# Kernel optimization log

Hardware: AMD Instinct MI355X
Metric: run time of the kernel (lower is better)

Reference implementation:

```python
import jax, jax.numpy as jnp
import numpy as np

N_NODES = 100000
N_EDGES = 600000
N_FEAT = 128


def setup_inputs() -> dict:
    key = jax.random.key(0)
    k1, k2, k3 = jax.random.split(key, 3)
    x = jax.random.normal(k1, (N_NODES, N_FEAT), dtype=jnp.float32)
    W = jax.random.normal(k2, (N_FEAT, N_FEAT), dtype=jnp.float32) / np.sqrt(N_FEAT)
    b = jnp.zeros((N_FEAT,), dtype=jnp.float32)
    edge_index = jax.random.randint(k3, (2, N_EDGES), 0, N_NODES, dtype=jnp.int64)
    return {"x": x, "W": W, "b": b, "edge_index": edge_index}


def reference(x, W, b, edge_index):
    # GCNConv: out = D^{-1/2} (A + I) D^{-1/2} (x @ W) + b, then ReLU
    n = x.shape[0]
    loop = jnp.arange(n, dtype=edge_index.dtype)
    src = jnp.concatenate([edge_index[0], loop])  # [E + N]
    dst = jnp.concatenate([edge_index[1], loop])  # [E + N]

    # degree of target nodes (includes self-loops)
    ones = jnp.ones(src.shape[0], dtype=x.dtype)
    deg = jax.ops.segment_sum(ones, dst, num_segments=n)  # [N]
    dinv = jnp.where(deg > 0, jax.lax.rsqrt(deg), 0.0)
    norm = dinv[src] * dinv[dst]  # [E + N]

    h = x @ W  # [N, F]
    msg = h[src] * norm[:, None]  # gather + scale, [E + N, F]
    agg = jax.ops.segment_sum(msg, dst, num_segments=n)  # scatter-add, [N, F]
    return jax.nn.relu(agg + b)
```

## Files before the change

kernel.cpp:

```cpp
#include <hip/hip_runtime.h>

#define NN 100000
#define NE 600000
#define F  128
#define CAP 32

#define NBLK   ((NN + 255) / 256)
#define GEMM_B ((NN + 127) / 128)
#define FILL_B ((NE + 2047) / 2048)

#define OFF_DEG  0
#define OFF_FLAG (960*1024)
#define OFF_WT   (1024*1024)
#define OFF_G    (2048*1024)
#define OFF_CSR  (28672*1024)

typedef __attribute__((ext_vector_type(8))) short bf16x8;
typedef __attribute__((ext_vector_type(16))) float f32x16;
typedef __attribute__((ext_vector_type(4)))  float f32x4;

__device__ inline unsigned short f2b(float f) {
    unsigned int u = __builtin_bit_cast(unsigned int, f);
    u += 0x7fffu + ((u >> 16) & 1u);
    return (unsigned short)(u >> 16);
}
__device__ inline float b_lo(unsigned int v) {
    return __builtin_bit_cast(float, v << 16);
}
__device__ inline float b_hi(unsigned int v) {
    return __builtin_bit_cast(float, v & 0xffff0000u);
}
__device__ inline void acc8(float* a, uint4 v, float d) {
    a[0] += b_lo(v.x) * d; a[1] += b_hi(v.x) * d;
    a[2] += b_lo(v.y) * d; a[3] += b_hi(v.y) * d;
    a[4] += b_lo(v.z) * d; a[5] += b_hi(v.z) * d;
    a[6] += b_lo(v.w) * d; a[7] += b_hi(v.w) * d;
}

__global__ __launch_bounds__(256) void k_init(const int* __restrict__ ei,
                                              const float* __restrict__ W,
                                              int* __restrict__ deg,
                                              int* __restrict__ flag,
                                              unsigned short* __restrict__ pb) {
    int i = blockIdx.x * 256 + threadIdx.x;
    if (i < NN) deg[i] = 0;
    if (i < F * F) {
        int j  = i & 7;
        int l  = (i >> 3) & 63;
        int tt = i >> 9;
        int k  = (tt >> 2) * 16 + ((l >> 5) << 3) + j;
        int n  = (tt & 3) * 32 + (l & 31);
        pb[i] = f2b(W[k * F + n]);
    }
    if (blockIdx.x == 0) {
        __shared__ int cnt;
        if (threadIdx.x == 0) cnt = 0;
        __syncthreads();
        if (ei[2 * threadIdx.x + 1] == 0) atomicAdd(&cnt, 1);
        __syncthreads();
        if (threadIdx.x == 0) *flag = (cnt > 128) ? 1 : 0;
    }
}

__global__ __launch_bounds__(256) void k_gemm_fill(const float* __restrict__ x,
                                                   const unsigned short* __restrict__ pb,
                                                   unsigned short* __restrict__ gb,
                                                   const int* __restrict__ ei,
                                                   const int* __restrict__ flag,
                                                   int* __restrict__ deg,
                                                   int* __restrict__ csr) {
    if (blockIdx.x < FILL_B) {
        const int base = blockIdx.x * 2048 + threadIdx.x;
        if (*flag) {
            const uint2* e64 = (const uint2*)ei;
#pragma unroll
            for (int i = 0; i < 8; ++i) {
                int e = base + i * 256;
                if (e < NE) {
                    int src = (int)e64[e].x;
                    int dst = (int)e64[NE + e].x;
                    int slot = atomicAdd(&deg[dst], 1);
                    if (slot < CAP) csr[slot * NN + dst] = src;
                }
            }
        } else {
#pragma unroll
            for (int i = 0; i < 8; ++i) {
                int e = base + i * 256;
                if (e < NE) {
                    int src = ei[e];
                    int dst = ei[NE + e];
                    int slot = atomicAdd(&deg[dst], 1);
                    if (slot < CAP) csr[slot * NN + dst] = src;
                }
            }
        }
        return;
    }

    __shared__ unsigned short xs[128 * 128];
    const int t    = threadIdx.x;
    const int row0 = (blockIdx.x - FILL_B) * 128;

#pragma unroll 4
    for (int it = 0; it < 16; ++it) {
        int r  = it * 8 + (t >> 5);
        int gr = min(row0 + r, NN - 1);
        float4 v = *(const float4*)(x + (long)gr * F + (t & 31) * 4);
        unsigned int lo = (unsigned int)f2b(v.x) | ((unsigned int)f2b(v.y) << 16);
        unsigned int hi = (unsigned int)f2b(v.z) | ((unsigned int)f2b(v.w) << 16);
        int bcol = ((t & 31) * 8) ^ ((r & 15) << 4);
        uint2 u; u.x = lo; u.y = hi;
        *(uint2*)((char*)xs + r * 256 + bcol) = u;
    }
    __syncthreads();

    const int w    = t >> 6;
    const int lane = t & 63;
    const int m    = lane & 31;
    const int half = lane >> 5;

    f32x16 acc[4];
#pragma unroll
    for (int nt = 0; nt < 4; ++nt)
#pragma unroll
        for (int j = 0; j < 16; ++j) acc[nt][j] = 0.f;

    const int r = 32 * w + m;
    const unsigned short* pw = pb + lane * 8;

#pragma unroll
    for (int kc = 0; kc < 8; ++kc) {
        int bcol = (kc * 32 + half * 16) ^ ((r & 15) << 4);
        bf16x8 a = *(const bf16x8*)((const char*)xs + r * 256 + bcol);
#pragma unroll
        for (int nt = 0; nt < 4; ++nt) {
            bf16x8 bfr = *(const bf16x8*)(pw + (kc * 4 + nt) * 512);
            acc[nt] = __builtin_amdgcn_mfma_f32_32x32x16_bf16(a, bfr, acc[nt], 0, 0, 0);
        }
    }
    __syncthreads();

    const int rbase = 32 * w + 4 * half;
#pragma unroll
    for (int nt = 0; nt < 4; ++nt) {
#pragma unroll
        for (int reg = 0; reg < 16; ++reg) {
            int row = rbase + (reg & 3) + 8 * (reg >> 2);
            int cb  = (nt * 32 + m) * 2;
            *(unsigned short*)((char*)xs + row * 256 + (cb ^ ((row & 15) << 4))) =
                f2b(acc[nt][reg]);
        }
    }
    __syncthreads();

#pragma unroll
    for (int p = 0; p < 8; ++p) {
        int row  = p * 16 + (t >> 4);
        int cb   = (t & 15) * 16;
        uint4 v  = *(const uint4*)((const char*)xs + row * 256 + (cb ^ ((row & 15) << 4)));
        int grow = row0 + row;
        if (grow < NN)
            *(uint4*)((char*)gb + (long)grow * 256 + cb) = v;
    }
}

__global__ __launch_bounds__(256) void k_gather(const int* __restrict__ deg,
                                                const int* __restrict__ csr,
                                                const unsigned short* __restrict__ gb,
                                                const float* __restrict__ b,
                                                float* __restrict__ out) {
    int n = blockIdx.x * 4 + (threadIdx.x >> 6);
    if (n >= NN) return;
    const int lane = threadIdx.x & 63;
    const int l16  = lane & 15;
    const int grp  = lane >> 4;
    const int dn   = deg[n];
    const int dnc  = min(dn, CAP);
    const float dvn = rsqrtf((float)(dn + 1));

    float a[8];
    if (grp == 0) {
        uint4 v = *(const uint4*)(gb + (long)n * F + l16 * 8);
        a[0] = b_lo(v.x) * dvn; a[1] = b_hi(v.x) * dvn;
        a[2] = b_lo(v.y) * dvn; a[3] = b_hi(v.y) * dvn;
        a[4] = b_lo(v.z) * dvn; a[5] = b_hi(v.z) * dvn;
        a[6] = b_lo(v.w) * dvn; a[7] = b_hi(v.w) * dvn;
    } else {
#pragma unroll
        for (int j = 0; j < 8; ++j) a[j] = 0.f;
    }

    const int p0 = grp, p1 = grp + 4, p2 = grp + 8, p3 = grp + 12;
    int s0 = n, s1 = n, s2 = n, s3 = n;
    if (p0 < dnc) s0 = csr[p0 * NN + n];
    if (p1 < dnc) s1 = csr[p1 * NN + n];
    if (p2 < dnc) s2 = csr[p2 * NN + n];
    if (p3 < dnc) s3 = csr[p3 * NN + n];
    uint4 z; z.x = z.y = z.z = z.w = 0u;
    uint4 v0 = z, v1 = z, v2 = z, v3 = z;
    if (p0 < dnc) v0 = *(const uint4*)(gb + (long)s0 * F + l16 * 8);
    if (p1 < dnc) v1 = *(const uint4*)(gb + (long)s1 * F + l16 * 8);
    if (p2 < dnc) v2 = *(const uint4*)(gb + (long)s2 * F + l16 * 8);
    if (p3 < dnc) v3 = *(const uint4*)(gb + (long)s3 * F + l16 * 8);
    float d0 = rsqrtf((float)(deg[s0] + 1));
    float d1 = rsqrtf((float)(deg[s1] + 1));
    float d2 = rsqrtf((float)(deg[s2] + 1));
    float d3 = rsqrtf((float)(deg[s3] + 1));
    acc8(a, v0, d0);
    acc8(a, v1, d1);
    acc8(a, v2, d2);
    acc8(a, v3, d3);

    for (int p = grp + 16; p < dnc; p += 4) {
        int s = csr[p * NN + n];
        float d = rsqrtf((float)(deg[s] + 1));
        uint4 v = *(const uint4*)(gb + (long)s * F + l16 * 8);
        acc8(a, v, d);
    }

#pragma unroll
    for (int j = 0; j < 8; ++j) {
        a[j] += __shfl_xor(a[j], 16);
        a[j] += __shfl_xor(a[j], 32);
    }

    if (grp == 0) {
        float4 b0 = *(const float4*)(b + l16 * 8);
        float4 b1 = *(const float4*)(b + l16 * 8 + 4);
        f32x4 o0, o1;
        o0[0] = fmaxf(a[0] * dvn + b0.x, 0.f);
        o0[1] = fmaxf(a[1] * dvn + b0.y, 0.f);
        o0[2] = fmaxf(a[2] * dvn + b0.z, 0.f);
        o0[3] = fmaxf(a[3] * dvn + b0.w, 0.f);
        o1[0] = fmaxf(a[4] * dvn + b1.x, 0.f);
        o1[1] = fmaxf(a[5] * dvn + b1.y, 0.f);
        o1[2] = fmaxf(a[6] * dvn + b1.z, 0.f);
        o1[3] = fmaxf(a[7] * dvn + b1.w, 0.f);
        long obase = (long)n * F + l16 * 8;
        __builtin_nontemporal_store(o0, (f32x4*)(out + obase));
        __builtin_nontemporal_store(o1, (f32x4*)(out + obase + 4));
    }
}

extern "C" void kernel_launch(void* const* d_in, const int* in_sizes, int n_in,
                              void* d_out, int out_size, void* d_ws, size_t ws_size,
                              hipStream_t stream) {
    const float* x  = (const float*)d_in[0];
    const float* W  = (const float*)d_in[1];
    const float* b  = (const float*)d_in[2];
    const int*   ei = (const int*)d_in[3];
    float* out = (float*)d_out;

    char* ws = (char*)d_ws;
    int*            deg  = (int*)(ws + OFF_DEG);
    int*            flag = (int*)(ws + OFF_FLAG);
    unsigned short* pb   = (unsigned short*)(ws + OFF_WT);
    unsigned short* gb   = (unsigned short*)(ws + OFF_G);
    int*            csr  = (int*)(ws + OFF_CSR);

    k_init<<<NBLK, 256, 0, stream>>>(ei, W, deg, flag, pb);
    k_gemm_fill<<<FILL_B + GEMM_B, 256, 0, stream>>>(x, pb, gb, ei, flag, deg, csr);
    k_gather<<<(NN + 3) / 4, 256, 0, stream>>>(deg, csr, gb, b, out);
}
```

Baseline: 179.0 us.

## Fuse init, gemm/fill and gather into one cooperative persistent kernel

Merges the three kernel launches into a single cooperative kernel that uses grid-wide syncs between the init, fill/GEMM and gather phases. Blocks loop over virtual block indices in a persistent style, with the grid sized from an occupancy query. The goal is to remove launch gaps and tail drain between kernels. The cost is grid.sync overhead, a grid capped by occupancy (256 per CU assumed) and possibly lower latency hiding in the gather phase. It falls back to the three-kernel path if the cooperative launch fails.

```diff
diff --git a/kernel.cpp b/kernel.cpp
--- a/kernel.cpp
+++ b/kernel.cpp
@@ -1,4 +1,7 @@
 #include <hip/hip_runtime.h>
+#include <hip/hip_cooperative_groups.h>
+
+namespace cg = cooperative_groups;
 
 #define NN 100000
 #define NE 600000
@@ -8,6 +11,8 @@
 #define NBLK   ((NN + 255) / 256)
 #define GEMM_B ((NN + 127) / 128)
 #define FILL_B ((NE + 2047) / 2048)
+#define PH1_B  (FILL_B + GEMM_B)
+#define GATH_B ((NN + 3) / 4)
 
 #define OFF_DEG  0
 #define OFF_FLAG (960*1024)
@@ -37,14 +42,13 @@
     a[6] += b_lo(v.w) * d; a[7] += b_hi(v.w) * d;
 }
 
-__global__ __launch_bounds__(256) void k_init(const int* __restrict__ ei,
-                                              const float* __restrict__ W,
-                                              int* __restrict__ deg,
-                                              int* __restrict__ flag,
-                                              unsigned short* __restrict__ pb) {
-    int i = blockIdx.x * 256 + threadIdx.x;
-    if (i < NN) deg[i] = 0;
-    if (i < F * F) {
+
+__device__ __forceinline__ void init_body(const float* __restrict__ W,
+                                          int* __restrict__ deg,
+                                          unsigned short* __restrict__ pb,
+                                          int gtid, int gstride) {
+    for (int i = gtid; i < NN; i += gstride) deg[i] = 0;
+    for (int i = gtid; i < F * F; i += gstride) {
         int j  = i & 7;
         int l  = (i >> 3) & 63;
         int tt = i >> 9;
@@ -52,55 +56,44 @@
         int n  = (tt & 3) * 32 + (l & 31);
         pb[i] = f2b(W[k * F + n]);
     }
-    if (blockIdx.x == 0) {
-        __shared__ int cnt;
-        if (threadIdx.x == 0) cnt = 0;
-        __syncthreads();
-        if (ei[2 * threadIdx.x + 1] == 0) atomicAdd(&cnt, 1);
-        __syncthreads();
-        if (threadIdx.x == 0) *flag = (cnt > 128) ? 1 : 0;
-    }
-}
-
-__global__ __launch_bounds__(256) void k_gemm_fill(const float* __restrict__ x,
-                                                   const unsigned short* __restrict__ pb,
-                                                   unsigned short* __restrict__ gb,
-                                                   const int* __restrict__ ei,
-                                                   const int* __restrict__ flag,
-                                                   int* __restrict__ deg,
-                                                   int* __restrict__ csr) {
-    if (blockIdx.x < FILL_B) {
-        const int base = blockIdx.x * 2048 + threadIdx.x;
-        if (*flag) {
-            const uint2* e64 = (const uint2*)ei;
-#pragma unroll
-            for (int i = 0; i < 8; ++i) {
-                int e = base + i * 256;
-                if (e < NE) {
-                    int src = (int)e64[e].x;
-                    int dst = (int)e64[NE + e].x;
-                    int slot = atomicAdd(&deg[dst], 1);
-                    if (slot < CAP) csr[slot * NN + dst] = src;
-                }
+}
+
+__device__ __forceinline__ void fill_body(int fb, const int* __restrict__ ei,
+                                          int f64, int* __restrict__ deg,
+                                          int* __restrict__ csr) {
+    const int base = fb * 2048 + threadIdx.x;
+    if (f64) {
+        const uint2* e64 = (const uint2*)ei;
+#pragma unroll
+        for (int i = 0; i < 8; ++i) {
+            int e = base + i * 256;
+            if (e < NE) {
+                int src = (int)e64[e].x;
+                int dst = (int)e64[NE + e].x;
+                int slot = atomicAdd(&deg[dst], 1);
+                if (slot < CAP) csr[slot * NN + dst] = src;
             }
-        } else {
-#pragma unroll
-            for (int i = 0; i < 8; ++i) {
-                int e = base + i * 256;
-                if (e < NE) {
-                    int src = ei[e];
-                    int dst = ei[NE + e];
-                    int slot = atomicAdd(&deg[dst], 1);
-                    if (slot < CAP) csr[slot * NN + dst] = src;
-                }
+        }
+    } else {
+#pragma unroll
+        for (int i = 0; i < 8; ++i) {
+            int e = base + i * 256;
+            if (e < NE) {
+                int src = ei[e];
+                int dst = ei[NE + e];
+                int slot = atomicAdd(&deg[dst], 1);
+                if (slot < CAP) csr[slot * NN + dst] = src;
             }
         }
-        return;
-    }
-
-    __shared__ unsigned short xs[128 * 128];
+    }
+}
+
+__device__ __forceinline__ void gemm_body(int gbi, const float* __restrict__ x,
+                                          const unsigned short* __restrict__ pb,
+                                          unsigned short* __restrict__ gb,
+                                          unsigned short* xs) {
     const int t    = threadIdx.x;
-    const int row0 = (blockIdx.x - FILL_B) * 128;
+    const int row0 = gbi * 128;
 
 #pragma unroll 4
     for (int it = 0; it < 16; ++it) {
@@ -163,14 +156,15 @@
         if (grow < NN)
             *(uint4*)((char*)gb + (long)grow * 256 + cb) = v;
     }
-}
-
-__global__ __launch_bounds__(256) void k_gather(const int* __restrict__ deg,
-                                                const int* __restrict__ csr,
-                                                const unsigned short* __restrict__ gb,
-                                                const float* __restrict__ b,
-                                                float* __restrict__ out) {
-    int n = blockIdx.x * 4 + (threadIdx.x >> 6);
+    __syncthreads();
+}
+
+__device__ __forceinline__ void gather_body(int vb, const int* __restrict__ deg,
+                                            const int* __restrict__ csr,
+                                            const unsigned short* __restrict__ gb,
+                                            const float* __restrict__ b,
+                                            float* __restrict__ out) {
+    int n = vb * 4 + (threadIdx.x >> 6);
     if (n >= NN) return;
     const int lane = threadIdx.x & 63;
     const int l16  = lane & 15;
@@ -243,6 +237,79 @@
     }
 }
 
+__global__ __launch_bounds__(256) void k_fused(const float* __restrict__ x,
+                                               const float* __restrict__ W,
+                                               const float* __restrict__ b,
+                                               const int* __restrict__ ei,
+                                               float* __restrict__ out,
+                                               int* __restrict__ deg,
+                                               int* __restrict__ flag,
+                                               unsigned short* __restrict__ pb,
+                                               unsigned short* __restrict__ gb,
+                                               int* __restrict__ csr) {
+    __shared__ unsigned short xs[128 * 128];
+    cg::grid_group grid = cg::this_grid();
+    const int gtid    = blockIdx.x * 256 + threadIdx.x;
+    const int gstride = gridDim.x * 256;
+
+    init_body(W, deg, pb, gtid, gstride);
+    if (blockIdx.x == 0) {
+        __shared__ int cnt;
+        if (threadIdx.x == 0) cnt = 0;
+        __syncthreads();
+        if (ei[2 * threadIdx.x + 1] == 0) atomicAdd(&cnt, 1);
+        __syncthreads();
+        if (threadIdx.x == 0) *flag = (cnt > 128) ? 1 : 0;
+    }
+    grid.sync();
+
+    const int f64 = *flag;
+    for (int v = blockIdx.x; v < PH1_B; v += gridDim.x) {
+        if (v < FILL_B) fill_body(v, ei, f64, deg, csr);
+        else            gemm_body(v - FILL_B, x, pb, gb, xs);
+    }
+    grid.sync();
+
+    for (int v = blockIdx.x; v < GATH_B; v += gridDim.x)
+        gather_body(v, deg, csr, gb, b, out);
+}
+
+__global__ __launch_bounds__(256) void k_init(const int* __restrict__ ei,
+                                              const float* __restrict__ W,
+                                              int* __restrict__ deg,
+                                              int* __restrict__ flag,
+                                              unsigned short* __restrict__ pb) {
+    init_body(W, deg, pb, blockIdx.x * 256 + threadIdx.x, NBLK * 256);
+    if (blockIdx.x == 0) {
+        __shared__ int cnt;
+        if (threadIdx.x == 0) cnt = 0;
+        __syncthreads();
+        if (ei[2 * threadIdx.x + 1] == 0) atomicAdd(&cnt, 1);
+        __syncthreads();
+        if (threadIdx.x == 0) *flag = (cnt > 128) ? 1 : 0;
+    }
+}
+
+__global__ __launch_bounds__(256) void k_gemm_fill(const float* __restrict__ x,
+                                                   const unsigned short* __restrict__ pb,
+                                                   unsigned short* __restrict__ gb,
+                                                   const int* __restrict__ ei,
+                                                   const int* __restrict__ flag,
+                                                   int* __restrict__ deg,
+                                                   int* __restrict__ csr) {
+    __shared__ unsigned short xs[128 * 128];
+    if (blockIdx.x < FILL_B) fill_body(blockIdx.x, ei, *flag, deg, csr);
+    else                     gemm_body(blockIdx.x - FILL_B, x, pb, gb, xs);
+}
+
+__global__ __launch_bounds__(256) void k_gather(const int* __restrict__ deg,
+                                                const int* __restrict__ csr,
+                                                const unsigned short* __restrict__ gb,
+                                                const float* __restrict__ b,
+                                                float* __restrict__ out) {
+    gather_body(blockIdx.x, deg, csr, gb, b, out);
+}
+
 extern "C" void kernel_launch(void* const* d_in, const int* in_sizes, int n_in,
                               void* d_out, int out_size, void* d_ws, size_t ws_size,
                               hipStream_t stream) {
@@ -259,7 +326,32 @@
     unsigned short* gb   = (unsigned short*)(ws + OFF_G);
     int*            csr  = (int*)(ws + OFF_CSR);
 
-    k_init<<<NBLK, 256, 0, stream>>>(ei, W, deg, flag, pb);
-    k_gemm_fill<<<FILL_B + GEMM_B, 256, 0, stream>>>(x, pb, gb, ei, flag, deg, csr);
-    k_gather<<<(NN + 3) / 4, 256, 0, stream>>>(deg, csr, gb, b, out);
-}
+    static int coop_grid = -2;
+    if (coop_grid == -2) {
+        int maxb = 0;
+        if (hipOccupancyMaxActiveBlocksPerMultiprocessor(&maxb, k_fused, 256, 0)
+                == hipSuccess && maxb > 0) {
+            long g = (long)maxb * 256;
+            coop_grid = (int)(g > PH1_B ? PH1_B : g);
+        } else {
+            coop_grid = -1;
+        }
+    }
+
+    bool ok = false;
+    if (coop_grid > 0) {
+        void* args[] = {(void*)&x, (void*)&W, (void*)&b, (void*)&ei, (void*)&out,
+                        (void*)&deg, (void*)&flag, (void*)&pb, (void*)&gb, (void*)&csr};
+        ok = hipLaunchCooperativeKernel((const void*)k_fused, dim3(coop_grid),
+                                        dim3(256), args, 0, stream) == hipSuccess;
+        if (!ok) {
+            (void)hipGetLastError();
+            coop_grid = -1;
+        }
+    }
+    if (!ok) {
+        k_init<<<NBLK, 256, 0, stream>>>(ei, W, deg, flag, pb);
+        k_gemm_fill<<<FILL_B + GEMM_B, 256, 0, stream>>>(x, pb, gb, ei, flag, deg, csr);
+        k_gather<<<GATH_B, 256, 0, stream>>>(deg, csr, gb, b, out);
+    }
+}
```

Result: slower. 384.1 us (+114.6%).
